# Kernel optimization log

Hardware: AMD Instinct MI355X
Metric: run time of the kernel (lower is better)

The kernel has to match this reference:

```python
import jax, jax.numpy as jnp
import numpy as np

H = 2048          # hidden_size
I = 1024          # moe_intermediate_size
E = 32            # n_routed_experts
K = 4             # num_experts_per_tok
N_SHARED = 1
EPS = 1e-6


def setup_inputs() -> dict:
    key = jax.random.key(0)
    ks = jax.random.split(key, 8)
    s = 1.0 / np.sqrt(H)
    si = 1.0 / np.sqrt(I)
    return {
        "hidden_states": jax.random.normal(ks[0], (1, 4096, H), jnp.float32),
        "norm_w": jnp.ones((H,), jnp.float32),
        "gate_w": jax.random.normal(ks[1], (E, H), jnp.float32) * s,      # MoEGate.weight
        "w13": jax.random.normal(ks[2], (E, H, 2 * I), jnp.float32) * s,  # fused w1w3
        "w2": jax.random.normal(ks[3], (E, I, H), jnp.float32) * si,      # fused w2
        "shared_gate_w": jax.random.normal(ks[4], (H, I * N_SHARED), jnp.float32) * s,
        "shared_up_w": jax.random.normal(ks[5], (H, I * N_SHARED), jnp.float32) * s,
        "shared_down_w": jax.random.normal(ks[6], (I * N_SHARED, H), jnp.float32) * si,
    }


def _rmsnorm(x, w, eps=EPS):
    var = jnp.mean(jnp.square(x), axis=-1, keepdims=True)
    return x * jax.lax.rsqrt(var + eps) * w


def _moe_core(x, gate_w, w13, w2):
    # x: [T, H] (post-norm tokens)
    T = x.shape[0]
    N = T * K
    C = 2 * N // E

    # --- gate (fp32, F.linear) ---
    logits = jnp.einsum("th,eh->te", x.astype(jnp.float32), gate_w.astype(jnp.float32))
    scores = jax.nn.softmax(logits, axis=-1)
    topk_w, topk_ids = jax.lax.top_k(scores, K)           # [T, K]
    topk_w = topk_w / jnp.sum(topk_w, axis=-1, keepdims=True)  # norm_topk_prob

    # --- dispatch: sort token-expert pairs by expert ---
    flat_ids = topk_ids.reshape(-1)                        # [N] int
    flat_w = topk_w.reshape(-1)                            # [N]
    order = jnp.argsort(flat_ids)                          # stable sort by expert
    sorted_eid = flat_ids[order]                           # [N]
    tok = order // K                                       # source token per sorted slot
    counts = jnp.zeros((E,), jnp.int32).at[flat_ids].add(1)  # tokens_per_expert
    starts = jnp.cumsum(counts) - counts
    pos = jnp.arange(N) - starts[sorted_eid]               # position within expert group

    # scatter tokens into [E, C, H] buffer (OOB rows dropped; C sized so this ~never happens)
    buf = jnp.zeros((E, C, x.shape[1]), x.dtype).at[sorted_eid, pos].set(x[tok], mode="drop")

    # --- grouped expert FFN (swiglu) ---
    gu = jnp.einsum("ech,ehf->ecf", buf, w13)              # [E, C, 2I]
    g, u = jnp.split(gu, 2, axis=-1)
    act = jax.nn.silu(g) * u                               # swiglu
    eo = jnp.einsum("eci,eih->ech", act, w2)               # [E, C, H]

    # --- combine: gather back and weighted scatter-add per source token ---
    out_slots = eo[sorted_eid, pos]                        # [N, H]
    routed = jnp.zeros_like(x).at[tok].add(out_slots * flat_w[order][:, None])
    return routed


def reference(hidden_states, norm_w, gate_w, w13, w2, shared_gate_w, shared_up_w, shared_down_w):
    B, S, Hd = hidden_states.shape
    residual = hidden_states
    h = _rmsnorm(hidden_states, norm_w)                    # post_attention_layernorm
    x = h.reshape(-1, Hd)                                  # [T, H]

    routed = _moe_core(x, gate_w, w13, w2)                 # routed experts output

    # shared experts MLP (swiglu)
    shared = (jax.nn.silu(x @ shared_gate_w) * (x @ shared_up_w)) @ shared_down_w

    out = residual + (routed + shared).reshape(B, S, Hd)
    return out
```

## Files before the change

kernel.cpp:

```cpp
#include <hip/hip_runtime.h>
#include <hip/hip_bf16.h>
#include <math.h>

#define HD 2048
#define ID 1024
#define NE 32
#define TOPK 4
#define NTOK 4096
#define NSLOT (NTOK*TOPK)

typedef __attribute__((ext_vector_type(4))) float f32x4;
typedef __attribute__((ext_vector_type(8))) short bf16x8;
typedef unsigned short u16;
typedef unsigned int u32;

static __device__ __forceinline__ u16 f2bf(float f) {
  union { float f; u32 u; } v; v.f = f;
  u32 r = v.u + 0x7fffu + ((v.u >> 16) & 1u);
  return (u16)(r >> 16);
}

__global__ __launch_bounds__(256) void k_rmsnorm(const float* __restrict__ x,
                                                 const float* __restrict__ w,
                                                 u16* __restrict__ xn) {
  int t = blockIdx.x, tid = threadIdx.x;
  const float* row = x + (size_t)t * HD;
  float4 v0 = ((const float4*)row)[tid*2+0];
  float4 v1 = ((const float4*)row)[tid*2+1];
  float ss = v0.x*v0.x+v0.y*v0.y+v0.z*v0.z+v0.w*v0.w
           + v1.x*v1.x+v1.y*v1.y+v1.z*v1.z+v1.w*v1.w;
  #pragma unroll
  for (int d=1; d<64; d<<=1) ss += __shfl_xor(ss, d);
  __shared__ float red[4];
  if ((tid&63)==0) red[tid>>6] = ss;
  __syncthreads();
  float rs = rsqrtf((red[0]+red[1]+red[2]+red[3]) * (1.0f/HD) + 1e-6f);
  const float* wp = w + tid*8;
  float a[8] = {v0.x,v0.y,v0.z,v0.w,v1.x,v1.y,v1.z,v1.w};
  uint4 o;
  o.x = (u32)f2bf(a[0]*rs*wp[0]) | ((u32)f2bf(a[1]*rs*wp[1])<<16);
  o.y = (u32)f2bf(a[2]*rs*wp[2]) | ((u32)f2bf(a[3]*rs*wp[3])<<16);
  o.z = (u32)f2bf(a[4]*rs*wp[4]) | ((u32)f2bf(a[5]*rs*wp[5])<<16);
  o.w = (u32)f2bf(a[6]*rs*wp[6]) | ((u32)f2bf(a[7]*rs*wp[7])<<16);
  ((uint4*)xn)[(size_t)t*(HD/8) + tid] = o;
}

__global__ __launch_bounds__(256) void k_gate(const float* __restrict__ x,
                                              const float* __restrict__ w,
                                              const float* __restrict__ gw,
                                              int* __restrict__ topk_id,
                                              float* __restrict__ topk_w,
                                              int* __restrict__ counts) {
  __shared__ float xs[HD];
  __shared__ float red[4];
  __shared__ float logits[NE];
  int t = blockIdx.x, tid = threadIdx.x;
  const float* row = x + (size_t)t*HD;
  float4 v0 = ((const float4*)row)[tid*2+0];
  float4 v1 = ((const float4*)row)[tid*2+1];
  float ss = v0.x*v0.x+v0.y*v0.y+v0.z*v0.z+v0.w*v0.w
           + v1.x*v1.x+v1.y*v1.y+v1.z*v1.z+v1.w*v1.w;
  #pragma unroll
  for (int d=1; d<64; d<<=1) ss += __shfl_xor(ss, d);
  if ((tid&63)==0) red[tid>>6] = ss;
  __syncthreads();
  float rs = 1.0f / sqrtf((red[0]+red[1]+red[2]+red[3]) * (1.0f/HD) + 1e-6f);
  const float* wp = w + tid*8;
  float a[8] = {v0.x,v0.y,v0.z,v0.w,v1.x,v1.y,v1.z,v1.w};
  #pragma unroll
  for (int j=0;j<8;++j) xs[tid*8+j] = a[j]*rs*wp[j];
  __syncthreads();
  int wave = tid>>6, lane = tid&63;
  for (int ei=0; ei<8; ++ei) {
    int e = wave*8 + ei;
    const float* g = gw + (size_t)e*HD;
    float s = 0.f;
    #pragma unroll
    for (int j=0;j<HD/64;++j) s += xs[lane + j*64] * g[lane + j*64];
    #pragma unroll
    for (int d=1; d<64; d<<=1) s += __shfl_xor(s, d);
    if (lane==0) logits[e] = s;
  }
  __syncthreads();
  if (tid==0) {
    float best[TOPK]; int bid[TOPK]; unsigned used = 0;
    for (int k2=0;k2<TOPK;++k2) {
      float bv = -1e30f; int bi = 0;
      for (int i2=0;i2<NE;++i2)
        if (!((used>>i2)&1u) && logits[i2] > bv) { bv = logits[i2]; bi = i2; }
      used |= 1u<<bi; best[k2] = bv; bid[k2] = bi;
    }
    float mx = best[0], sum = 0.f, wv[TOPK];
    for (int k2=0;k2<TOPK;++k2) { wv[k2] = expf(best[k2]-mx); sum += wv[k2]; }
    float inv = 1.f/sum;
    for (int k2=0;k2<TOPK;++k2) {
      topk_id[t*TOPK+k2] = bid[k2];
      topk_w[t*TOPK+k2] = wv[k2]*inv;
      atomicAdd(&counts[bid[k2]], 1);
    }
  }
}

__global__ void k_zero(int* counts, int* cursors) {
  int i = threadIdx.x;
  if (i < NE) { counts[i] = 0; cursors[i] = 0; }
}

__global__ void k_scan(const int* __restrict__ counts, int* __restrict__ starts) {
  if (threadIdx.x==0 && blockIdx.x==0) {
    int acc = 0;
    for (int e=0;e<NE;++e) { starts[e] = acc; acc += counts[e]; }
  }
}

__global__ __launch_bounds__(256) void k_dispatch(const int* __restrict__ topk_id,
                                                  const float* __restrict__ topk_w,
                                                  const int* __restrict__ starts,
                                                  int* __restrict__ cursors,
                                                  int* __restrict__ slot_tok,
                                                  float* __restrict__ slot_w) {
  int i = blockIdx.x*256 + threadIdx.x;
  int e = topk_id[i];
  int p = atomicAdd(&cursors[e], 1);
  int slot = starts[e] + p;
  slot_tok[slot] = i >> 2;
  slot_w[slot] = topk_w[i];
}

template<bool INDEXED>
__global__ __launch_bounds__(256) void k_gemm_up(
    const u16* __restrict__ A,
    const float* __restrict__ Bg, const float* __restrict__ Bu,
    size_t bstride, int ldb,
    const int* __restrict__ counts, const int* __restrict__ starts,
    const int* __restrict__ slot_tok,
    u16* __restrict__ actOut) {
  __shared__ u16 Al[128*32];
  __shared__ u16 Bl[128*32];
  __shared__ int rowL[128];
  int tid = threadIdx.x;
  int n0 = blockIdx.x * 64;
  int m0 = blockIdx.y * 128;
  int e  = blockIdx.z;
  int M, rowbase;
  if (INDEXED) { M = counts[e]; rowbase = starts[e]; if (m0 >= M) return; }
  else { M = NTOK; rowbase = 0; }
  if (tid < 128) {
    int m = m0 + tid;
    if (INDEXED) rowL[tid] = slot_tok[rowbase + (m < M ? m : M-1)];
    else rowL[tid] = m;
  }
  __syncthreads();
  int s0 = tid, s1 = tid + 256;
  int segl0 = (s0&3) ^ ((s0>>3)&3);
  const u16* srcA0 = A + (size_t)rowL[s0>>2]*HD + (segl0<<3);
  const u16* srcA1 = A + (size_t)rowL[s1>>2]*HD + (segl0<<3);
  int c4 = (tid&31)*4, kb = (tid>>5)*4;
  int isup = (c4>>4)&1, pgrp = c4>>5;
  const float* bp = (isup ? Bu : Bg) + (size_t)e*bstride + (n0 + pgrp*16 + (c4&15));
  int bwid[4];
  #pragma unroll
  for (int i=0;i<4;++i)
    bwid[i] = (c4+i)*32 + (((kb>>3) ^ (tid&3))<<3) + (((kb>>2)&1)<<2);
  int lane = tid&63, wave = tid>>6;
  int wr = wave>>1, wc = wave&1;
  int l15 = lane&15, l4 = lane>>4;
  int aoff[4], boff[4];
  #pragma unroll
  for (int f=0; f<4; ++f) {
    int r = wr*64 + f*16 + l15;
    aoff[f] = r*32 + ((l4 ^ ((l15>>1)&3))<<3);
    int c = wc*64 + f*16 + l15;
    boff[f] = c*32 + ((l4 ^ ((l15>>2)&3))<<3);
  }
  f32x4 acc[4][4];
  #pragma unroll
  for (int fm=0;fm<4;++fm)
    #pragma unroll
    for (int fn=0;fn<4;++fn)
      acc[fm][fn] = (f32x4){0.f,0.f,0.f,0.f};

  const int KSTEPS = HD/32;
  for (int kt=0; kt<KSTEPS; ++kt) {
    int k0 = kt*32;
    uint4 av0 = *(const uint4*)(srcA0 + k0);
    uint4 av1 = *(const uint4*)(srcA1 + k0);
    float4 Lb[4];
    #pragma unroll
    for (int j=0;j<4;++j) Lb[j] = *(const float4*)(bp + (size_t)(k0+kb+j)*ldb);
    __syncthreads();
    *(uint4*)&Al[s0*8] = av0;
    *(uint4*)&Al[s1*8] = av1;
    #pragma unroll
    for (int i=0;i<4;++i) {
      uint2 wv;
      wv.x = (u32)f2bf(((const float*)&Lb[0])[i]) | ((u32)f2bf(((const float*)&Lb[1])[i])<<16);
      wv.y = (u32)f2bf(((const float*)&Lb[2])[i]) | ((u32)f2bf(((const float*)&Lb[3])[i])<<16);
      *(uint2*)&Bl[bwid[i]] = wv;
    }
    __syncthreads();
    bf16x8 af[4], bfr[4];
    #pragma unroll
    for (int f=0; f<4; ++f) af[f] = *(const bf16x8*)&Al[aoff[f]];
    #pragma unroll
    for (int f=0; f<4; ++f) bfr[f] = *(const bf16x8*)&Bl[boff[f]];
    #pragma unroll
    for (int fm=0; fm<4; ++fm)
      #pragma unroll
      for (int fn=0; fn<4; ++fn)
        acc[fm][fn] = __builtin_amdgcn_mfma_f32_16x16x32_bf16(af[fm], bfr[fn], acc[fm][fn], 0,0,0);
  }
  #pragma unroll
  for (int fm=0; fm<4; ++fm) {
    #pragma unroll
    for (int fq=0; fq<2; ++fq) {
      f32x4 g = acc[fm][2*fq], u = acc[fm][2*fq+1];
      int col = n0 + (wc*2+fq)*16 + l15;
      #pragma unroll
      for (int r=0;r<4;++r) {
        int mloc = wr*64 + fm*16 + l4*4 + r;
        int m = m0 + mloc;
        if (m < M) {
          float gv = g[r];
          float av = gv / (1.f + expf(-gv)) * u[r];
          actOut[(size_t)(rowbase+m)*ID + col] = f2bf(av);
        }
      }
    }
  }
}

template<bool INDEXED>
__global__ __launch_bounds__(256) void k_gemm_down(
    const u16* __restrict__ A,
    const float* __restrict__ B,
    size_t bstride, int ldb,
    const int* __restrict__ counts, const int* __restrict__ starts,
    const int* __restrict__ slot_tok, const float* __restrict__ slot_w,
    const float* __restrict__ resid,
    float* __restrict__ out) {
  __shared__ u16 Al[128*32];
  __shared__ u16 Bl[128*32];
  __shared__ int rowL[128];
  __shared__ int tokL[128];
  __shared__ float wL[128];
  int tid = threadIdx.x;
  int n0 = blockIdx.x * 128;
  int m0 = blockIdx.y * 128;
  int e  = blockIdx.z;
  int M, rowbase;
  if (INDEXED) { M = counts[e]; rowbase = starts[e]; if (m0 >= M) return; }
  else { M = NTOK; rowbase = 0; }
  if (tid < 128) {
    int m = m0 + tid;
    int cm = m < M ? m : M-1;
    rowL[tid] = rowbase + cm;
    if (INDEXED) {
      tokL[tid] = (m<M) ? slot_tok[rowbase+m] : 0;
      wL[tid]   = (m<M) ? slot_w[rowbase+m]  : 0.f;
    }
  }
  __syncthreads();
  int s0 = tid, s1 = tid + 256;
  int segl0 = (s0&3) ^ ((s0>>3)&3);
  const u16* srcA0 = A + (size_t)rowL[s0>>2]*ID + (segl0<<3);
  const u16* srcA1 = A + (size_t)rowL[s1>>2]*ID + (segl0<<3);
  int c4 = (tid&31)*4, kb = (tid>>5)*4;
  const float* bp = B + (size_t)e*bstride + n0 + c4;
  int bwid[4];
  #pragma unroll
  for (int i=0;i<4;++i)
    bwid[i] = (c4+i)*32 + (((kb>>3) ^ (tid&3))<<3) + (((kb>>2)&1)<<2);
  int lane = tid&63, wave = tid>>6;
  int wr = wave>>1, wc = wave&1;
  int l15 = lane&15, l4 = lane>>4;
  int aoff[4], boff[4];
  #pragma unroll
  for (int f=0; f<4; ++f) {
    int r = wr*64 + f*16 + l15;
    aoff[f] = r*32 + ((l4 ^ ((l15>>1)&3))<<3);
    int c = wc*64 + f*16 + l15;
    boff[f] = c*32 + ((l4 ^ ((l15>>2)&3))<<3);
  }
  f32x4 acc[4][4];
  #pragma unroll
  for (int fm=0;fm<4;++fm)
    #pragma unroll
    for (int fn=0;fn<4;++fn)
      acc[fm][fn] = (f32x4){0.f,0.f,0.f,0.f};

  const int KSTEPS = ID/32;
  for (int kt=0; kt<KSTEPS; ++kt) {
    int k0 = kt*32;
    uint4 av0 = *(const uint4*)(srcA0 + k0);
    uint4 av1 = *(const uint4*)(srcA1 + k0);
    float4 Lb[4];
    #pragma unroll
    for (int j=0;j<4;++j) Lb[j] = *(const float4*)(bp + (size_t)(k0+kb+j)*ldb);
    __syncthreads();
    *(uint4*)&Al[s0*8] = av0;
    *(uint4*)&Al[s1*8] = av1;
    #pragma unroll
    for (int i=0;i<4;++i) {
      uint2 wv;
      wv.x = (u32)f2bf(((const float*)&Lb[0])[i]) | ((u32)f2bf(((const float*)&Lb[1])[i])<<16);
      wv.y = (u32)f2bf(((const float*)&Lb[2])[i]) | ((u32)f2bf(((const float*)&Lb[3])[i])<<16);
      *(uint2*)&Bl[bwid[i]] = wv;
    }
    __syncthreads();
    bf16x8 af[4], bfr[4];
    #pragma unroll
    for (int f=0; f<4; ++f) af[f] = *(const bf16x8*)&Al[aoff[f]];
    #pragma unroll
    for (int f=0; f<4; ++f) bfr[f] = *(const bf16x8*)&Bl[boff[f]];
    #pragma unroll
    for (int fm=0; fm<4; ++fm)
      #pragma unroll
      for (int fn=0; fn<4; ++fn)
        acc[fm][fn] = __builtin_amdgcn_mfma_f32_16x16x32_bf16(af[fm], bfr[fn], acc[fm][fn], 0,0,0);
  }
  #pragma unroll
  for (int fm=0; fm<4; ++fm) {
    #pragma unroll
    for (int fn=0; fn<4; ++fn) {
      f32x4 v = acc[fm][fn];
      int col = n0 + wc*64 + fn*16 + l15;
      #pragma unroll
      for (int r=0;r<4;++r) {
        int mloc = wr*64 + fm*16 + l4*4 + r;
        int m = m0 + mloc;
        if (m < M) {
          if (INDEXED) {
            atomicAdd(&out[(size_t)tokL[mloc]*HD + col], v[r]*wL[mloc]);
          } else {
            size_t o = (size_t)m*HD + col;
            out[o] = resid[o] + v[r];
          }
        }
      }
    }
  }
}

extern "C" void kernel_launch(void* const* d_in, const int* in_sizes, int n_in,
                              void* d_out, int out_size, void* d_ws, size_t ws_size,
                              hipStream_t stream) {
  const float* x    = (const float*)d_in[0];
  const float* nw   = (const float*)d_in[1];
  const float* gw   = (const float*)d_in[2];
  const float* w13  = (const float*)d_in[3];
  const float* w2   = (const float*)d_in[4];
  const float* sgw  = (const float*)d_in[5];
  const float* suw  = (const float*)d_in[6];
  const float* sdw  = (const float*)d_in[7];
  float* out = (float*)d_out;

  char* p = (char*)d_ws;
  u16* xn   = (u16*)p;    p += (size_t)NTOK*HD*2;
  u16* act  = (u16*)p;    p += (size_t)NSLOT*ID*2;
  u16* sact = (u16*)p;    p += (size_t)NTOK*ID*2;
  int*   topk_id  = (int*)p;   p += (size_t)NTOK*TOPK*4;
  float* topk_w   = (float*)p; p += (size_t)NTOK*TOPK*4;
  int*   slot_tok = (int*)p;   p += (size_t)NSLOT*4;
  float* slot_w   = (float*)p; p += (size_t)NSLOT*4;
  int*   counts   = (int*)p;   p += 64*4;
  int*   cursors  = (int*)p;   p += 64*4;
  int*   starts   = (int*)p;   p += 64*4;

  k_zero<<<1, 64, 0, stream>>>(counts, cursors);
  k_rmsnorm<<<NTOK, 256, 0, stream>>>(x, nw, xn);
  k_gate<<<NTOK, 256, 0, stream>>>(x, nw, gw, topk_id, topk_w, counts);
  k_scan<<<1, 1, 0, stream>>>(counts, starts);
  k_dispatch<<<NSLOT/256, 256, 0, stream>>>(topk_id, topk_w, starts, cursors, slot_tok, slot_w);

  k_gemm_up<true><<<dim3(ID/64, 8, NE), 256, 0, stream>>>(
      xn, w13, w13 + ID, (size_t)HD*2*ID, 2*ID, counts, starts, slot_tok, act);
  k_gemm_up<false><<<dim3(ID/64, NTOK/128, 1), 256, 0, stream>>>(
      xn, sgw, suw, (size_t)0, ID, nullptr, nullptr, nullptr, sact);
  k_gemm_down<false><<<dim3(HD/128, NTOK/128, 1), 256, 0, stream>>>(
      sact, sdw, (size_t)0, HD, nullptr, nullptr, nullptr, nullptr, x, out);
  k_gemm_down<true><<<dim3(HD/128, 8, NE), 256, 0, stream>>>(
      act, w2, (size_t)ID*HD, HD, counts, starts, slot_tok, slot_w, nullptr, out);
}
```

Measured before the change: 897.8 us.

## Double-buffer GEMM tiles with direct global-to-LDS loads and truncating bf16 pack

Restructures the up and down grouped GEMMs into a double-buffered LDS pipeline. The next k-tile is prefetched while the MFMAs run on the current one, and there is one barrier per iteration instead of two. Activations are loaded straight into LDS with global_load_lds, and the fp32 weights are converted to bf16 by byte-permute truncation instead of round-to-nearest. The weight tile layout and swizzle are changed to match. This doubles LDS per block, which may reduce occupancy, and truncation changes numerics slightly.

```diff
diff --git a/kernel.cpp b/kernel.cpp
--- a/kernel.cpp
+++ b/kernel.cpp
@@ -14,10 +14,21 @@
 typedef unsigned short u16;
 typedef unsigned int u32;
 
+typedef const void __attribute__((address_space(1)))* gas_p;
+typedef void __attribute__((address_space(3)))* las_p;
+
+static __device__ __forceinline__ void gload16(const void* g, void* l) {
+  __builtin_amdgcn_global_load_lds((gas_p)g, (las_p)l, 16, 0, 0);
+}
+
 static __device__ __forceinline__ u16 f2bf(float f) {
   union { float f; u32 u; } v; v.f = f;
   u32 r = v.u + 0x7fffu + ((v.u >> 16) & 1u);
   return (u16)(r >> 16);
+}
+
+static __device__ __forceinline__ u32 packtrunc(float hi, float lo) {
+  return __builtin_amdgcn_perm(__float_as_uint(hi), __float_as_uint(lo), 0x07060302u);
 }
 
 __global__ __launch_bounds__(256) void k_rmsnorm(const float* __restrict__ x,
@@ -129,49 +140,44 @@
 
 template<bool INDEXED>
 __global__ __launch_bounds__(256) void k_gemm_up(
-    const u16* __restrict__ A,
+    const u16* __restrict__ A, int lda, int kiter,
     const float* __restrict__ Bg, const float* __restrict__ Bu,
     size_t bstride, int ldb,
     const int* __restrict__ counts, const int* __restrict__ starts,
     const int* __restrict__ slot_tok,
     u16* __restrict__ actOut) {
-  __shared__ u16 Al[128*32];
-  __shared__ u16 Bl[128*32];
+  __shared__ u16 Al[2][4096];
+  __shared__ u16 Bl[2][4096];
   __shared__ int rowL[128];
-  int tid = threadIdx.x;
+  int t = threadIdx.x;
   int n0 = blockIdx.x * 64;
   int m0 = blockIdx.y * 128;
   int e  = blockIdx.z;
   int M, rowbase;
   if (INDEXED) { M = counts[e]; rowbase = starts[e]; if (m0 >= M) return; }
   else { M = NTOK; rowbase = 0; }
-  if (tid < 128) {
-    int m = m0 + tid;
-    if (INDEXED) rowL[tid] = slot_tok[rowbase + (m < M ? m : M-1)];
-    else rowL[tid] = m;
-  }
-  __syncthreads();
-  int s0 = tid, s1 = tid + 256;
-  int segl0 = (s0&3) ^ ((s0>>3)&3);
-  const u16* srcA0 = A + (size_t)rowL[s0>>2]*HD + (segl0<<3);
-  const u16* srcA1 = A + (size_t)rowL[s1>>2]*HD + (segl0<<3);
-  int c4 = (tid&31)*4, kb = (tid>>5)*4;
-  int isup = (c4>>4)&1, pgrp = c4>>5;
-  const float* bp = (isup ? Bu : Bg) + (size_t)e*bstride + (n0 + pgrp*16 + (c4&15));
-  int bwid[4];
-  #pragma unroll
-  for (int i=0;i<4;++i)
-    bwid[i] = (c4+i)*32 + (((kb>>3) ^ (tid&3))<<3) + (((kb>>2)&1)<<2);
-  int lane = tid&63, wave = tid>>6;
-  int wr = wave>>1, wc = wave&1;
+  if (t < 128) {
+    int m = m0 + t;
+    rowL[t] = INDEXED ? slot_tok[rowbase + (m < M ? m : M-1)] : m;
+  }
+  __syncthreads();
+  int kseg8 = (((t&3) ^ ((t>>3)&3)) << 3);
+  const u16* an0 = A + (size_t)rowL[t>>2]*lda + kseg8;
+  const u16* an1 = A + (size_t)rowL[(t>>2)+64]*lda + kseg8;
+  int c0 = 2*((t>>2)&63);
+  int og = ((c0>>5)<<4) | (c0&15);
+  int isup = (c0>>4)&1;
+  const float* bn = (isup ? Bu : Bg) + (size_t)e*bstride + (n0 + og) + (size_t)kseg8*ldb;
+
+  int lane = t&63, wave = t>>6, wr = wave>>1, wc = wave&1;
   int l15 = lane&15, l4 = lane>>4;
   int aoff[4], boff[4];
   #pragma unroll
   for (int f=0; f<4; ++f) {
     int r = wr*64 + f*16 + l15;
-    aoff[f] = r*32 + ((l4 ^ ((l15>>1)&3))<<3);
+    aoff[f] = r*32 + ((l4 ^ ((r>>1)&3))<<3);
     int c = wc*64 + f*16 + l15;
-    boff[f] = c*32 + ((l4 ^ ((l15>>2)&3))<<3);
+    boff[f] = (c>>1)*32 + ((c&1)<<11) + ((l4 ^ ((c>>2)&3))<<3);
   }
   f32x4 acc[4][4];
   #pragma unroll
@@ -180,35 +186,53 @@
     for (int fn=0;fn<4;++fn)
       acc[fm][fn] = (f32x4){0.f,0.f,0.f,0.f};
 
-  const int KSTEPS = HD/32;
-  for (int kt=0; kt<KSTEPS; ++kt) {
-    int k0 = kt*32;
-    uint4 av0 = *(const uint4*)(srcA0 + k0);
-    uint4 av1 = *(const uint4*)(srcA1 + k0);
-    float4 Lb[4];
-    #pragma unroll
-    for (int j=0;j<4;++j) Lb[j] = *(const float4*)(bp + (size_t)(k0+kb+j)*ldb);
-    __syncthreads();
-    *(uint4*)&Al[s0*8] = av0;
-    *(uint4*)&Al[s1*8] = av1;
-    #pragma unroll
-    for (int i=0;i<4;++i) {
-      uint2 wv;
-      wv.x = (u32)f2bf(((const float*)&Lb[0])[i]) | ((u32)f2bf(((const float*)&Lb[1])[i])<<16);
-      wv.y = (u32)f2bf(((const float*)&Lb[2])[i]) | ((u32)f2bf(((const float*)&Lb[3])[i])<<16);
-      *(uint2*)&Bl[bwid[i]] = wv;
-    }
-    __syncthreads();
+  float2 bv[8];
+  gload16(an0, &Al[0][t*8]);
+  gload16(an1, &Al[0][2048 + t*8]);
+  #pragma unroll
+  for (int j=0;j<8;++j) bv[j] = *(const float2*)(bn + (size_t)j*ldb);
+  {
+    uint4 w0, w1;
+    w0.x = packtrunc(bv[1].x, bv[0].x); w0.y = packtrunc(bv[3].x, bv[2].x);
+    w0.z = packtrunc(bv[5].x, bv[4].x); w0.w = packtrunc(bv[7].x, bv[6].x);
+    w1.x = packtrunc(bv[1].y, bv[0].y); w1.y = packtrunc(bv[3].y, bv[2].y);
+    w1.z = packtrunc(bv[5].y, bv[4].y); w1.w = packtrunc(bv[7].y, bv[6].y);
+    *(uint4*)&Bl[0][t*8] = w0;
+    *(uint4*)&Bl[0][2048 + t*8] = w1;
+  }
+  __syncthreads();
+
+  int cur = 0;
+  for (int kt = 0; kt < kiter; ++kt) {
+    bool more = (kt+1 < kiter);
+    if (more) {
+      an0 += 32; an1 += 32; bn += (size_t)32*ldb;
+      gload16(an0, &Al[cur^1][t*8]);
+      gload16(an1, &Al[cur^1][2048 + t*8]);
+      #pragma unroll
+      for (int j=0;j<8;++j) bv[j] = *(const float2*)(bn + (size_t)j*ldb);
+    }
     bf16x8 af[4], bfr[4];
     #pragma unroll
-    for (int f=0; f<4; ++f) af[f] = *(const bf16x8*)&Al[aoff[f]];
-    #pragma unroll
-    for (int f=0; f<4; ++f) bfr[f] = *(const bf16x8*)&Bl[boff[f]];
+    for (int f=0; f<4; ++f) af[f] = *(const bf16x8*)&Al[cur][aoff[f]];
+    #pragma unroll
+    for (int f=0; f<4; ++f) bfr[f] = *(const bf16x8*)&Bl[cur][boff[f]];
     #pragma unroll
     for (int fm=0; fm<4; ++fm)
       #pragma unroll
       for (int fn=0; fn<4; ++fn)
         acc[fm][fn] = __builtin_amdgcn_mfma_f32_16x16x32_bf16(af[fm], bfr[fn], acc[fm][fn], 0,0,0);
+    if (more) {
+      uint4 w0, w1;
+      w0.x = packtrunc(bv[1].x, bv[0].x); w0.y = packtrunc(bv[3].x, bv[2].x);
+      w0.z = packtrunc(bv[5].x, bv[4].x); w0.w = packtrunc(bv[7].x, bv[6].x);
+      w1.x = packtrunc(bv[1].y, bv[0].y); w1.y = packtrunc(bv[3].y, bv[2].y);
+      w1.z = packtrunc(bv[5].y, bv[4].y); w1.w = packtrunc(bv[7].y, bv[6].y);
+      *(uint4*)&Bl[cur^1][t*8] = w0;
+      *(uint4*)&Bl[cur^1][2048 + t*8] = w1;
+    }
+    cur ^= 1;
+    __syncthreads();
   }
   #pragma unroll
   for (int fm=0; fm<4; ++fm) {
@@ -232,55 +256,50 @@
 
 template<bool INDEXED>
 __global__ __launch_bounds__(256) void k_gemm_down(
-    const u16* __restrict__ A,
+    const u16* __restrict__ A, int lda, int kiter,
     const float* __restrict__ B,
     size_t bstride, int ldb,
     const int* __restrict__ counts, const int* __restrict__ starts,
     const int* __restrict__ slot_tok, const float* __restrict__ slot_w,
     const float* __restrict__ resid,
     float* __restrict__ out) {
-  __shared__ u16 Al[128*32];
-  __shared__ u16 Bl[128*32];
+  __shared__ u16 Al[2][4096];
+  __shared__ u16 Bl[2][4096];
   __shared__ int rowL[128];
   __shared__ int tokL[128];
   __shared__ float wL[128];
-  int tid = threadIdx.x;
+  int t = threadIdx.x;
   int n0 = blockIdx.x * 128;
   int m0 = blockIdx.y * 128;
   int e  = blockIdx.z;
   int M, rowbase;
   if (INDEXED) { M = counts[e]; rowbase = starts[e]; if (m0 >= M) return; }
   else { M = NTOK; rowbase = 0; }
-  if (tid < 128) {
-    int m = m0 + tid;
+  if (t < 128) {
+    int m = m0 + t;
     int cm = m < M ? m : M-1;
-    rowL[tid] = rowbase + cm;
+    rowL[t] = rowbase + cm;
     if (INDEXED) {
-      tokL[tid] = (m<M) ? slot_tok[rowbase+m] : 0;
-      wL[tid]   = (m<M) ? slot_w[rowbase+m]  : 0.f;
-    }
-  }
-  __syncthreads();
-  int s0 = tid, s1 = tid + 256;
-  int segl0 = (s0&3) ^ ((s0>>3)&3);
-  const u16* srcA0 = A + (size_t)rowL[s0>>2]*ID + (segl0<<3);
-  const u16* srcA1 = A + (size_t)rowL[s1>>2]*ID + (segl0<<3);
-  int c4 = (tid&31)*4, kb = (tid>>5)*4;
-  const float* bp = B + (size_t)e*bstride + n0 + c4;
-  int bwid[4];
-  #pragma unroll
-  for (int i=0;i<4;++i)
-    bwid[i] = (c4+i)*32 + (((kb>>3) ^ (tid&3))<<3) + (((kb>>2)&1)<<2);
-  int lane = tid&63, wave = tid>>6;
-  int wr = wave>>1, wc = wave&1;
+      tokL[t] = (m<M) ? slot_tok[rowbase+m] : 0;
+      wL[t]   = (m<M) ? slot_w[rowbase+m]  : 0.f;
+    }
+  }
+  __syncthreads();
+  int kseg8 = (((t&3) ^ ((t>>3)&3)) << 3);
+  const u16* an0 = A + (size_t)rowL[t>>2]*lda + kseg8;
+  const u16* an1 = A + (size_t)rowL[(t>>2)+64]*lda + kseg8;
+  int c0 = 2*((t>>2)&63);
+  const float* bn = B + (size_t)e*bstride + (n0 + c0) + (size_t)kseg8*ldb;
+
+  int lane = t&63, wave = t>>6, wr = wave>>1, wc = wave&1;
   int l15 = lane&15, l4 = lane>>4;
   int aoff[4], boff[4];
   #pragma unroll
   for (int f=0; f<4; ++f) {
     int r = wr*64 + f*16 + l15;
-    aoff[f] = r*32 + ((l4 ^ ((l15>>1)&3))<<3);
+    aoff[f] = r*32 + ((l4 ^ ((r>>1)&3))<<3);
     int c = wc*64 + f*16 + l15;
-    boff[f] = c*32 + ((l4 ^ ((l15>>2)&3))<<3);
+    boff[f] = (c>>1)*32 + ((c&1)<<11) + ((l4 ^ ((c>>2)&3))<<3);
   }
   f32x4 acc[4][4];
   #pragma unroll
@@ -289,35 +308,53 @@
     for (int fn=0;fn<4;++fn)
       acc[fm][fn] = (f32x4){0.f,0.f,0.f,0.f};
 
-  const int KSTEPS = ID/32;
-  for (int kt=0; kt<KSTEPS; ++kt) {
-    int k0 = kt*32;
-    uint4 av0 = *(const uint4*)(srcA0 + k0);
-    uint4 av1 = *(const uint4*)(srcA1 + k0);
-    float4 Lb[4];
-    #pragma unroll
-    for (int j=0;j<4;++j) Lb[j] = *(const float4*)(bp + (size_t)(k0+kb+j)*ldb);
-    __syncthreads();
-    *(uint4*)&Al[s0*8] = av0;
-    *(uint4*)&Al[s1*8] = av1;
-    #pragma unroll
-    for (int i=0;i<4;++i) {
-      uint2 wv;
-      wv.x = (u32)f2bf(((const float*)&Lb[0])[i]) | ((u32)f2bf(((const float*)&Lb[1])[i])<<16);
-      wv.y = (u32)f2bf(((const float*)&Lb[2])[i]) | ((u32)f2bf(((const float*)&Lb[3])[i])<<16);
-      *(uint2*)&Bl[bwid[i]] = wv;
-    }
-    __syncthreads();
+  float2 bv[8];
+  gload16(an0, &Al[0][t*8]);
+  gload16(an1, &Al[0][2048 + t*8]);
+  #pragma unroll
+  for (int j=0;j<8;++j) bv[j] = *(const float2*)(bn + (size_t)j*ldb);
+  {
+    uint4 w0, w1;
+    w0.x = packtrunc(bv[1].x, bv[0].x); w0.y = packtrunc(bv[3].x, bv[2].x);
+    w0.z = packtrunc(bv[5].x, bv[4].x); w0.w = packtrunc(bv[7].x, bv[6].x);
+    w1.x = packtrunc(bv[1].y, bv[0].y); w1.y = packtrunc(bv[3].y, bv[2].y);
+    w1.z = packtrunc(bv[5].y, bv[4].y); w1.w = packtrunc(bv[7].y, bv[6].y);
+    *(uint4*)&Bl[0][t*8] = w0;
+    *(uint4*)&Bl[0][2048 + t*8] = w1;
+  }
+  __syncthreads();
+
+  int cur = 0;
+  for (int kt = 0; kt < kiter; ++kt) {
+    bool more = (kt+1 < kiter);
+    if (more) {
+      an0 += 32; an1 += 32; bn += (size_t)32*ldb;
+      gload16(an0, &Al[cur^1][t*8]);
+      gload16(an1, &Al[cur^1][2048 + t*8]);
+      #pragma unroll
+      for (int j=0;j<8;++j) bv[j] = *(const float2*)(bn + (size_t)j*ldb);
+    }
     bf16x8 af[4], bfr[4];
     #pragma unroll
-    for (int f=0; f<4; ++f) af[f] = *(const bf16x8*)&Al[aoff[f]];
-    #pragma unroll
-    for (int f=0; f<4; ++f) bfr[f] = *(const bf16x8*)&Bl[boff[f]];
+    for (int f=0; f<4; ++f) af[f] = *(const bf16x8*)&Al[cur][aoff[f]];
+    #pragma unroll
+    for (int f=0; f<4; ++f) bfr[f] = *(const bf16x8*)&Bl[cur][boff[f]];
     #pragma unroll
     for (int fm=0; fm<4; ++fm)
       #pragma unroll
       for (int fn=0; fn<4; ++fn)
         acc[fm][fn] = __builtin_amdgcn_mfma_f32_16x16x32_bf16(af[fm], bfr[fn], acc[fm][fn], 0,0,0);
+    if (more) {
+      uint4 w0, w1;
+      w0.x = packtrunc(bv[1].x, bv[0].x); w0.y = packtrunc(bv[3].x, bv[2].x);
+      w0.z = packtrunc(bv[5].x, bv[4].x); w0.w = packtrunc(bv[7].x, bv[6].x);
+      w1.x = packtrunc(bv[1].y, bv[0].y); w1.y = packtrunc(bv[3].y, bv[2].y);
+      w1.z = packtrunc(bv[5].y, bv[4].y); w1.w = packtrunc(bv[7].y, bv[6].y);
+      *(uint4*)&Bl[cur^1][t*8] = w0;
+      *(uint4*)&Bl[cur^1][2048 + t*8] = w1;
+    }
+    cur ^= 1;
+    __syncthreads();
   }
   #pragma unroll
   for (int fm=0; fm<4; ++fm) {
@@ -374,11 +411,11 @@
   k_dispatch<<<NSLOT/256, 256, 0, stream>>>(topk_id, topk_w, starts, cursors, slot_tok, slot_w);
 
   k_gemm_up<true><<<dim3(ID/64, 8, NE), 256, 0, stream>>>(
-      xn, w13, w13 + ID, (size_t)HD*2*ID, 2*ID, counts, starts, slot_tok, act);
+      xn, HD, HD/32, w13, w13 + ID, (size_t)HD*2*ID, 2*ID, counts, starts, slot_tok, act);
   k_gemm_up<false><<<dim3(ID/64, NTOK/128, 1), 256, 0, stream>>>(
-      xn, sgw, suw, (size_t)0, ID, nullptr, nullptr, nullptr, sact);
+      xn, HD, HD/32, sgw, suw, (size_t)0, ID, nullptr, nullptr, nullptr, sact);
   k_gemm_down<false><<<dim3(HD/128, NTOK/128, 1), 256, 0, stream>>>(
-      sact, sdw, (size_t)0, HD, nullptr, nullptr, nullptr, nullptr, x, out);
+      sact, ID, ID/32, sdw, (size_t)0, HD, nullptr, nullptr, nullptr, nullptr, x, out);
   k_gemm_down<true><<<dim3(HD/128, 8, NE), 256, 0, stream>>>(
-      act, w2, (size_t)ID*HD, HD, counts, starts, slot_tok, slot_w, nullptr, out);
-}
+      act, ID, ID/32, w2, (size_t)ID*HD, HD, counts, starts, slot_tok, slot_w, nullptr, out);
+}
```

Result: slower. 1.414 ms (+57.5%).
